# Kernel tuning notes

Measured on AMD Instinct MI355X. Metric: run time of the kernel, lower is better.

## Reference

```python
import jax, jax.numpy as jnp
import numpy as np

N = 100000
E = 1600000
IN_F, HID, OUT_F = 256, 128, 64


def setup_inputs() -> dict:
    key = jax.random.key(0)
    k_x, k_e, k_w1, k_w2, k_b1, k_b2 = jax.random.split(key, 6)
    x = jax.random.normal(k_x, (N, IN_F), dtype=jnp.float32)
    edge_index = jax.random.randint(k_e, (2, E), 0, N, dtype=jnp.int32)
    # GCNConv params: lin has no bias in PyG; separate additive bias per layer.
    W1 = jax.random.normal(k_w1, (IN_F, HID), dtype=jnp.float32) / np.sqrt(IN_F)
    b1 = jax.random.normal(k_b1, (HID,), dtype=jnp.float32) * 0.01
    W2 = jax.random.normal(k_w2, (HID, OUT_F), dtype=jnp.float32) / np.sqrt(HID)
    b2 = jax.random.normal(k_b2, (OUT_F,), dtype=jnp.float32) * 0.01
    return {"x": x, "edge_index": edge_index, "W1": W1, "b1": b1, "W2": W2, "b2": b2}


def _gcn_norm(edge_index, num_nodes):
    # add self loops (improved=False -> weight 1.0), symmetric normalization
    loop = jnp.arange(num_nodes, dtype=edge_index.dtype)
    src = jnp.concatenate([edge_index[0], loop])
    dst = jnp.concatenate([edge_index[1], loop])
    w = jnp.ones(src.shape[0], dtype=jnp.float32)
    deg = jax.ops.segment_sum(w, dst, num_segments=num_nodes)
    dinv = jnp.where(deg > 0, jax.lax.rsqrt(deg), 0.0)
    norm = dinv[src] * w * dinv[dst]
    return src, dst, norm


def _gcn_layer(h, W, b, src, dst, norm, num_nodes):
    h = h @ W                               # [N, out]
    msg = h[src] * norm[:, None]            # [E+N, out] gather + scale
    out = jax.ops.segment_sum(msg, dst, num_segments=num_nodes)  # scatter-add
    return out + b


def reference(x, edge_index, W1, b1, W2, b2):
    # dropout is identity in eval mode
    src, dst, norm = _gcn_norm(edge_index, N)
    h = _gcn_layer(x, W1, b1, src, dst, norm, N)
    h = jax.nn.relu(h)
    out = _gcn_layer(h, W2, b2, src, dst, norm, N)
    return out
```

## Files before the change

### kernel.cpp

```cpp
#include <hip/hip_runtime.h>
#include <hip/hip_bf16.h>

#define N_NODES 100000
#define N_EDGES 1600000
#define IN_FEAT 256
#define HID_F   128
#define OUT_FT  64

#define NBUK   256
#define NPB    391
#define BUKCAP 8192
#define EPB    4096
#define G_BIN  ((N_EDGES + EPB - 1) / EPB)
#define G_GEMM ((N_NODES + 63) / 64)
#define G_CAST ((IN_FEAT * HID_F + HID_F * OUT_FT + 255) / 256)
#define G_AGG  ((N_NODES + 7) / 8)

typedef unsigned short u16;
typedef __attribute__((ext_vector_type(8))) unsigned short u16x8;
typedef __attribute__((ext_vector_type(8))) short short8;
typedef __attribute__((ext_vector_type(4))) float f32x4;

static __device__ inline u16 f2bf(float f) {
    __hip_bfloat16 h = __float2bfloat16(f);
    return *reinterpret_cast<u16*>(&h);
}
static __device__ inline float bf2f(u16 u) {
    union { unsigned u; float f; } c;
    c.u = ((unsigned)u) << 16;
    return c.f;
}


__global__ __launch_bounds__(256) void k_bin(const int* __restrict__ srcA,
                                             const int* __restrict__ dstA,
                                             int* __restrict__ gcur, int2* __restrict__ pairs,
                                             const float* __restrict__ W1,
                                             const float* __restrict__ W2,
                                             u16* __restrict__ W1t, u16* __restrict__ W2t) {
    if (blockIdx.x >= G_BIN) {
        int idx = (blockIdx.x - G_BIN) * 256 + threadIdx.x;
        if (idx < IN_FEAT * HID_F) {
            int k = idx / HID_F, n = idx % HID_F;
            W1t[n * IN_FEAT + k] = f2bf(W1[idx]);
        } else {
            int e2 = idx - IN_FEAT * HID_F;
            if (e2 < HID_F * OUT_FT) {
                int k = e2 / OUT_FT, n = e2 % OUT_FT;
                W2t[n * HID_F + k] = f2bf(W2[e2]);
            }
        }
        return;
    }
    __shared__ int lh[NBUK];
    int t = threadIdx.x;
    int e0 = blockIdx.x * EPB;
    if (t < NBUK) lh[t] = 0;
    __syncthreads();
#pragma unroll
    for (int i = 0; i < EPB / 256; i++) {
        int e = e0 + i * 256 + t;
        if (e < N_EDGES) atomicAdd(&lh[dstA[e] / NPB], 1);
    }
    __syncthreads();
    if (t < NBUK) {
        int c = lh[t];
        lh[t] = atomicAdd(&gcur[t], c);
    }
    __syncthreads();
#pragma unroll
    for (int i = 0; i < EPB / 256; i++) {
        int e = e0 + i * 256 + t;
        if (e < N_EDGES) {
            int d = dstA[e];
            int b = d / NPB;
            int p = atomicAdd(&lh[b], 1);
            if (p < BUKCAP) pairs[(size_t)b * BUKCAP + p] = make_int2(srcA[e], d);
        }
    }
}


__global__ __launch_bounds__(256) void k_fillB(const int2* __restrict__ pairs,
                                               const int* __restrict__ gcnt,
                                               int* __restrict__ offsets,
                                               float* __restrict__ dinv,
                                               int* __restrict__ csr) {
    __shared__ int hist[NPB];
    __shared__ int sm[256];
    __shared__ int s_ebase;
    int b = blockIdx.x, t = threadIdx.x;
    int nbase = b * NPB;
    int nn = min(NPB, N_NODES - nbase);

    int gv = gcnt[t];
    sm[t] = gv;
    __syncthreads();
    for (int o = 1; o < 256; o <<= 1) {
        int u = (t >= o) ? sm[t - o] : 0;
        __syncthreads();
        sm[t] += u;
        __syncthreads();
    }
    if (t == b) s_ebase = sm[t] - gv;
    __syncthreads();
    int ebase = s_ebase;
    int cnt = gcnt[b];
    const int2* pb = pairs + (size_t)b * BUKCAP;

    for (int i = t; i < NPB; i += 256) hist[i] = 0;
    __syncthreads();
    for (int i = t; i < cnt; i += 256) atomicAdd(&hist[pb[i].y - nbase], 1);
    __syncthreads();

    int base2 = t * 2;
    int c0 = (base2 < NPB) ? hist[base2] : 0;
    int c1 = (base2 + 1 < NPB) ? hist[base2 + 1] : 0;
    int s = c0 + c1;
    __syncthreads();
    sm[t] = s;
    __syncthreads();
    for (int o = 1; o < 256; o <<= 1) {
        int u = (t >= o) ? sm[t - o] : 0;
        __syncthreads();
        sm[t] += u;
        __syncthreads();
    }
    int run = ebase + sm[t] - s;
    __syncthreads();
    int cc[2] = {c0, c1};
#pragma unroll
    for (int q = 0; q < 2; q++) {
        int n = base2 + q;
        if (n < nn) {
            int g = nbase + n;
            offsets[g] = run;
            dinv[g] = rsqrtf((float)(cc[q] + 1));
            hist[n] = run;
            run += cc[q];
        }
    }
    __syncthreads();
    for (int i = t; i < cnt; i += 256) {
        int2 e = pb[i];
        int p = atomicAdd(&hist[e.y - nbase], 1);
        csr[p] = e.x;
    }
    if (b == NBUK - 1 && t == 0) offsets[N_NODES] = N_EDGES;
}


__global__ __launch_bounds__(256) void k_gemm1(const float* __restrict__ A,
                                               const u16* __restrict__ Bt,
                                               const float* __restrict__ dinv,
                                               u16* __restrict__ C) {
    __shared__ u16 As[2][64][40];
    __shared__ u16 Bs[2][128][40];
    int tid = threadIdx.x;
    int wv = tid >> 6, lane = tid & 63;
    int m16 = lane & 15, quad = lane >> 4;
    int row0 = blockIdx.x * 64;

    int ar = tid >> 2, aq = tid & 3;
    int br = tid >> 1, bh = tid & 1;
    int arow_g = row0 + ar;
    if (arow_g >= N_NODES) arow_g = N_NODES - 1;
    const float* ap = &A[(size_t)arow_g * IN_FEAT + aq * 8];
    const u16*   bp = &Bt[(size_t)br * IN_FEAT + bh * 16];

    f32x4 acc[8];
#pragma unroll
    for (int j = 0; j < 8; j++) acc[j] = (f32x4)(0.f);

    {
        f32x4 a0 = *(const f32x4*)&ap[0];
        f32x4 a1 = *(const f32x4*)&ap[4];
        u16x8 b0 = *(const u16x8*)&bp[0];
        u16x8 b1 = *(const u16x8*)&bp[8];
        u16x8 av;
#pragma unroll
        for (int j = 0; j < 4; j++) { av[j] = f2bf(a0[j]); av[4 + j] = f2bf(a1[j]); }
        *(u16x8*)&As[0][ar][aq * 8] = av;
        *(u16x8*)&Bs[0][br][bh * 16] = b0;
        *(u16x8*)&Bs[0][br][bh * 16 + 8] = b1;
    }

#pragma unroll
    for (int s = 0; s < 8; s++) {
        const int buf = s & 1;
        f32x4 na0, na1; u16x8 nb0, nb1;
        if (s + 1 < 8) {
            int k0 = (s + 1) * 32;
            na0 = *(const f32x4*)&ap[k0];
            na1 = *(const f32x4*)&ap[k0 + 4];
            nb0 = *(const u16x8*)&bp[k0];
            nb1 = *(const u16x8*)&bp[k0 + 8];
        }
        __syncthreads();
        short8 af = *(const short8*)&As[buf][wv * 16 + m16][quad * 8];
#pragma unroll
        for (int ct = 0; ct < 8; ct++) {
            short8 bf = *(const short8*)&Bs[buf][16 * ct + m16][quad * 8];
            acc[ct] = __builtin_amdgcn_mfma_f32_16x16x32_bf16(af, bf, acc[ct], 0, 0, 0);
        }
        if (s + 1 < 8) {
            u16x8 av;
#pragma unroll
            for (int j = 0; j < 4; j++) { av[j] = f2bf(na0[j]); av[4 + j] = f2bf(na1[j]); }
            *(u16x8*)&As[buf ^ 1][ar][aq * 8] = av;
            *(u16x8*)&Bs[buf ^ 1][br][bh * 16] = nb0;
            *(u16x8*)&Bs[buf ^ 1][br][bh * 16 + 8] = nb1;
        }
    }

#pragma unroll
    for (int r4 = 0; r4 < 4; r4++) {
        int grow = row0 + wv * 16 + quad * 4 + r4;
        if (grow < N_NODES) {
            float dv = dinv[grow];
#pragma unroll
            for (int ct = 0; ct < 8; ct++)
                C[(size_t)grow * HID_F + 16 * ct + m16] = f2bf(acc[ct][r4] * dv);
        }
    }
}


__global__ __launch_bounds__(256) void k_gemm2(const u16* __restrict__ A,
                                               const u16* __restrict__ Bt,
                                               const float* __restrict__ dinv,
                                               u16* __restrict__ C) {
    __shared__ u16 As[2][64][40];
    __shared__ u16 Bs[2][64][40];
    int tid = threadIdx.x;
    int wv = tid >> 6, lane = tid & 63;
    int m16 = lane & 15, quad = lane >> 4;
    int row0 = blockIdx.x * 64;

    int ar = tid >> 2, aq = tid & 3;
    int arow_g = row0 + ar;
    if (arow_g >= N_NODES) arow_g = N_NODES - 1;
    const u16* ap = &A[(size_t)arow_g * HID_F + aq * 8];
    const u16* bp = &Bt[(size_t)ar * HID_F + aq * 8];

    f32x4 acc[4];
#pragma unroll
    for (int j = 0; j < 4; j++) acc[j] = (f32x4)(0.f);

    {
        u16x8 a0 = *(const u16x8*)&ap[0];
        u16x8 b0 = *(const u16x8*)&bp[0];
        *(u16x8*)&As[0][ar][aq * 8] = a0;
        *(u16x8*)&Bs[0][ar][aq * 8] = b0;
    }

#pragma unroll
    for (int s = 0; s < 4; s++) {
        const int buf = s & 1;
        u16x8 na, nb;
        if (s + 1 < 4) {
            int k0 = (s + 1) * 32;
            na = *(const u16x8*)&ap[k0];
            nb = *(const u16x8*)&bp[k0];
        }
        __syncthreads();
        short8 af = *(const short8*)&As[buf][wv * 16 + m16][quad * 8];
#pragma unroll
        for (int ct = 0; ct < 4; ct++) {
            short8 bf = *(const short8*)&Bs[buf][16 * ct + m16][quad * 8];
            acc[ct] = __builtin_amdgcn_mfma_f32_16x16x32_bf16(af, bf, acc[ct], 0, 0, 0);
        }
        if (s + 1 < 4) {
            *(u16x8*)&As[buf ^ 1][ar][aq * 8] = na;
            *(u16x8*)&Bs[buf ^ 1][ar][aq * 8] = nb;
        }
    }

#pragma unroll
    for (int r4 = 0; r4 < 4; r4++) {
        int grow = row0 + wv * 16 + quad * 4 + r4;
        if (grow < N_NODES) {
            float dv = dinv[grow];
#pragma unroll
            for (int ct = 0; ct < 4; ct++)
                C[(size_t)grow * OUT_FT + 16 * ct + m16] = f2bf(acc[ct][r4] * dv);
        }
    }
}


__global__ __launch_bounds__(256) void k_agg1(const u16* __restrict__ hs,
                                              const int* __restrict__ offsets,
                                              const int* __restrict__ csr,
                                              const float* __restrict__ dinv,
                                              const float* __restrict__ b,
                                              u16* __restrict__ out) {
    int wave = threadIdx.x >> 6;
    int lane = threadIdx.x & 63;
    int half = lane >> 5;
    int node = blockIdx.x * 8 + wave * 2 + half;
    if (node >= N_NODES) return;
    int gl = lane & 31;
    int g = gl >> 4;
    int fl = gl & 15;
    const int fo = fl * 8;
    int beg = offsets[node], end = offsets[node + 1];

    float accA[8], accB[8];
#pragma unroll
    for (int i = 0; i < 8; i++) { accA[i] = 0.f; accB[i] = 0.f; }

    int j = beg;
    for (; j + 8 <= end; j += 8) {
        int s0 = csr[j + g];
        int s1 = csr[j + 2 + g];
        int s2 = csr[j + 4 + g];
        int s3 = csr[j + 6 + g];
        u16x8 r0 = *(const u16x8*)&hs[(size_t)s0 * HID_F + fo];
        u16x8 r1 = *(const u16x8*)&hs[(size_t)s1 * HID_F + fo];
        u16x8 r2 = *(const u16x8*)&hs[(size_t)s2 * HID_F + fo];
        u16x8 r3 = *(const u16x8*)&hs[(size_t)s3 * HID_F + fo];
#pragma unroll
        for (int i = 0; i < 8; i++) {
            accA[i] += bf2f(r0[i]) + bf2f(r1[i]);
            accB[i] += bf2f(r2[i]) + bf2f(r3[i]);
        }
    }
    if (j + 4 <= end) {
        int s0 = csr[j + g];
        int s1 = csr[j + 2 + g];
        u16x8 r0 = *(const u16x8*)&hs[(size_t)s0 * HID_F + fo];
        u16x8 r1 = *(const u16x8*)&hs[(size_t)s1 * HID_F + fo];
#pragma unroll
        for (int i = 0; i < 8; i++) accA[i] += bf2f(r0[i]) + bf2f(r1[i]);
        j += 4;
    }
    for (; j < end; j += 2) {
        int idx = j + g;
        if (idx < end) {
            int s = csr[idx];
            u16x8 r0 = *(const u16x8*)&hs[(size_t)s * HID_F + fo];
#pragma unroll
            for (int i = 0; i < 8; i++) accB[i] += bf2f(r0[i]);
        }
    }
#pragma unroll
    for (int i = 0; i < 8; i++) {
        float v = accA[i] + accB[i];
        v += __shfl_xor(v, 16, 64);
        accA[i] = v;
    }
    if (g == 0) {
        u16x8 sr = *(const u16x8*)&hs[(size_t)node * HID_F + fo];
        float dv = dinv[node];
        f32x4 b0 = *(const f32x4*)&b[fo];
        f32x4 b1 = *(const f32x4*)&b[fo + 4];
        u16x8 o;
#pragma unroll
        for (int i = 0; i < 4; i++) {
            o[i]     = f2bf(fmaxf(dv * (accA[i]     + bf2f(sr[i]))     + b0[i], 0.f));
            o[4 + i] = f2bf(fmaxf(dv * (accA[4 + i] + bf2f(sr[4 + i])) + b1[i], 0.f));
        }
        *(u16x8*)&out[(size_t)node * HID_F + fo] = o;
    }
}


__global__ __launch_bounds__(256) void k_agg2(const u16* __restrict__ hs,
                                              const int* __restrict__ offsets,
                                              const int* __restrict__ csr,
                                              const float* __restrict__ dinv,
                                              const float* __restrict__ b,
                                              float* __restrict__ out) {
    int wave = threadIdx.x >> 6;
    int lane = threadIdx.x & 63;
    int half = lane >> 5;
    int node = blockIdx.x * 8 + wave * 2 + half;
    if (node >= N_NODES) return;
    int gl = lane & 31;
    int g = gl >> 3;
    int fl = gl & 7;
    const int fo = fl * 8;
    int beg = offsets[node], end = offsets[node + 1];

    float accA[8], accB[8];
#pragma unroll
    for (int i = 0; i < 8; i++) { accA[i] = 0.f; accB[i] = 0.f; }

    int j = beg;
    for (; j + 16 <= end; j += 16) {
        int s0 = csr[j + g];
        int s1 = csr[j + 4 + g];
        int s2 = csr[j + 8 + g];
        int s3 = csr[j + 12 + g];
        u16x8 r0 = *(const u16x8*)&hs[(size_t)s0 * OUT_FT + fo];
        u16x8 r1 = *(const u16x8*)&hs[(size_t)s1 * OUT_FT + fo];
        u16x8 r2 = *(const u16x8*)&hs[(size_t)s2 * OUT_FT + fo];
        u16x8 r3 = *(const u16x8*)&hs[(size_t)s3 * OUT_FT + fo];
#pragma unroll
        for (int i = 0; i < 8; i++) {
            accA[i] += bf2f(r0[i]) + bf2f(r1[i]);
            accB[i] += bf2f(r2[i]) + bf2f(r3[i]);
        }
    }
    if (j + 8 <= end) {
        int s0 = csr[j + g];
        int s1 = csr[j + 4 + g];
        u16x8 r0 = *(const u16x8*)&hs[(size_t)s0 * OUT_FT + fo];
        u16x8 r1 = *(const u16x8*)&hs[(size_t)s1 * OUT_FT + fo];
#pragma unroll
        for (int i = 0; i < 8; i++) accA[i] += bf2f(r0[i]) + bf2f(r1[i]);
        j += 8;
    }
    for (; j < end; j += 4) {
        int idx = j + g;
        if (idx < end) {
            int s = csr[idx];
            u16x8 r0 = *(const u16x8*)&hs[(size_t)s * OUT_FT + fo];
#pragma unroll
            for (int i = 0; i < 8; i++) accB[i] += bf2f(r0[i]);
        }
    }
#pragma unroll
    for (int i = 0; i < 8; i++) {
        float v = accA[i] + accB[i];
        v += __shfl_xor(v, 8, 64);
        v += __shfl_xor(v, 16, 64);
        accA[i] = v;
    }
    if (g == 0) {
        u16x8 sr = *(const u16x8*)&hs[(size_t)node * OUT_FT + fo];
        float dv = dinv[node];
        f32x4 b0 = *(const f32x4*)&b[fo];
        f32x4 b1 = *(const f32x4*)&b[fo + 4];
        f32x4 o0, o1;
#pragma unroll
        for (int i = 0; i < 4; i++) {
            o0[i] = dv * (accA[i]     + bf2f(sr[i]))     + b0[i];
            o1[i] = dv * (accA[4 + i] + bf2f(sr[4 + i])) + b1[i];
        }
        *(f32x4*)&out[(size_t)node * OUT_FT + fo] = o0;
        *(f32x4*)&out[(size_t)node * OUT_FT + fo + 4] = o1;
    }
}


extern "C" void kernel_launch(void* const* d_in, const int* in_sizes, int n_in,
                              void* d_out, int out_size, void* d_ws, size_t ws_size,
                              hipStream_t stream) {
    const float* x  = (const float*)d_in[0];
    const int*   ei = (const int*)d_in[1];
    const float* W1 = (const float*)d_in[2];
    const float* b1 = (const float*)d_in[3];
    const float* W2 = (const float*)d_in[4];
    const float* b2 = (const float*)d_in[5];
    float* out = (float*)d_out;

    char* ws = (char*)d_ws;
    int*   offsets = (int*)(ws + 0);
    float* dinv    = (float*)(ws + 400512);
    int*   csr     = (int*)(ws + 800512);
    u16*   W1t     = (u16*)(ws + 7200512);
    u16*   W2t     = (u16*)(ws + 7266048);
    int*   gcur    = (int*)(ws + 7282432);
    u16*   hs1     = (u16*)(ws + 7284608);
    u16*   a1      = (u16*)(ws + 32884608);
    int2*  pairs   = (int2*)(ws + 32884608);
    u16*   hs2     = hs1;

    const int* srcA = ei;
    const int* dstA = ei + N_EDGES;

    hipMemsetAsync(gcur, 0, NBUK * sizeof(int), stream);

    k_bin<<<G_BIN + G_CAST, 256, 0, stream>>>(srcA, dstA, gcur, pairs, W1, W2, W1t, W2t);
    k_fillB<<<NBUK, 256, 0, stream>>>(pairs, gcur, offsets, dinv, csr);

    k_gemm1<<<G_GEMM, 256, 0, stream>>>(x, W1t, dinv, hs1);
    k_agg1<<<G_AGG, 256, 0, stream>>>(hs1, offsets, csr, dinv, b1, a1);
    k_gemm2<<<G_GEMM, 256, 0, stream>>>(a1, W2t, dinv, hs2);
    k_agg2<<<G_AGG, 256, 0, stream>>>(hs2, offsets, csr, dinv, b2, out);
}
```

Before: 338.2 us.

## Fuse layer-1 aggregation with layer-2 GEMM via shared-memory tile

```diff
diff --git a/kernel.cpp b/kernel.cpp
--- a/kernel.cpp
+++ b/kernel.cpp
@@ -226,53 +226,107 @@
 }
 
 
-__global__ __launch_bounds__(256) void k_gemm2(const u16* __restrict__ A,
-                                               const u16* __restrict__ Bt,
-                                               const float* __restrict__ dinv,
-                                               u16* __restrict__ C) {
-    __shared__ u16 As[2][64][40];
-    __shared__ u16 Bs[2][64][40];
-    int tid = threadIdx.x;
-    int wv = tid >> 6, lane = tid & 63;
-    int m16 = lane & 15, quad = lane >> 4;
+__global__ __launch_bounds__(256) void k_agg1gemm2(const u16* __restrict__ hs,
+                                                   const int* __restrict__ offsets,
+                                                   const int* __restrict__ csr,
+                                                   const float* __restrict__ dinv,
+                                                   const float* __restrict__ b1v,
+                                                   const u16* __restrict__ W2t,
+                                                   u16* __restrict__ hs2) {
+    __shared__ u16 As[4][65][40];
+    int t = threadIdx.x;
+    int wave = t >> 6;
+    int lane = t & 63;
+    int half = lane >> 5;
     int row0 = blockIdx.x * 64;
 
-    int ar = tid >> 2, aq = tid & 3;
-    int arow_g = row0 + ar;
-    if (arow_g >= N_NODES) arow_g = N_NODES - 1;
-    const u16* ap = &A[(size_t)arow_g * HID_F + aq * 8];
-    const u16* bp = &Bt[(size_t)ar * HID_F + aq * 8];
-
+    int gl = lane & 31;
+    int g = gl >> 4;
+    int fl = gl & 15;
+    const int fo = fl * 8;
+
+#pragma unroll 1
+    for (int sweep = 0; sweep < 8; sweep++) {
+        int nl = sweep * 8 + wave * 2 + half;
+        int node = row0 + nl;
+        if (node < N_NODES) {
+            int beg = offsets[node], end = offsets[node + 1];
+
+            float accA[8], accB[8];
+#pragma unroll
+            for (int i = 0; i < 8; i++) { accA[i] = 0.f; accB[i] = 0.f; }
+
+            int j = beg;
+            for (; j + 8 <= end; j += 8) {
+                int s0 = csr[j + g];
+                int s1 = csr[j + 2 + g];
+                int s2 = csr[j + 4 + g];
+                int s3 = csr[j + 6 + g];
+                u16x8 r0 = *(const u16x8*)&hs[(size_t)s0 * HID_F + fo];
+                u16x8 r1 = *(const u16x8*)&hs[(size_t)s1 * HID_F + fo];
+                u16x8 r2 = *(const u16x8*)&hs[(size_t)s2 * HID_F + fo];
+                u16x8 r3 = *(const u16x8*)&hs[(size_t)s3 * HID_F + fo];
+#pragma unroll
+                for (int i = 0; i < 8; i++) {
+                    accA[i] += bf2f(r0[i]) + bf2f(r1[i]);
+                    accB[i] += bf2f(r2[i]) + bf2f(r3[i]);
+                }
+            }
+            if (j + 4 <= end) {
+                int s0 = csr[j + g];
+                int s1 = csr[j + 2 + g];
+                u16x8 r0 = *(const u16x8*)&hs[(size_t)s0 * HID_F + fo];
+                u16x8 r1 = *(const u16x8*)&hs[(size_t)s1 * HID_F + fo];
+#pragma unroll
+                for (int i = 0; i < 8; i++) accA[i] += bf2f(r0[i]) + bf2f(r1[i]);
+                j += 4;
+            }
+            for (; j < end; j += 2) {
+                int idx = j + g;
+                if (idx < end) {
+                    int s = csr[idx];
+                    u16x8 r0 = *(const u16x8*)&hs[(size_t)s * HID_F + fo];
+#pragma unroll
+                    for (int i = 0; i < 8; i++) accB[i] += bf2f(r0[i]);
+                }
+            }
+#pragma unroll
+            for (int i = 0; i < 8; i++) {
+                float v = accA[i] + accB[i];
+                v += __shfl_xor(v, 16, 64);
+                accA[i] = v;
+            }
+            if (g == 0) {
+                u16x8 sr = *(const u16x8*)&hs[(size_t)node * HID_F + fo];
+                float dv = dinv[node];
+                f32x4 b0 = *(const f32x4*)&b1v[fo];
+                f32x4 b1q = *(const f32x4*)&b1v[fo + 4];
+                u16x8 o;
+#pragma unroll
+                for (int i = 0; i < 4; i++) {
+                    o[i]     = f2bf(fmaxf(dv * (accA[i]     + bf2f(sr[i]))     + b0[i], 0.f));
+                    o[4 + i] = f2bf(fmaxf(dv * (accA[4 + i] + bf2f(sr[4 + i])) + b1q[i], 0.f));
+                }
+                int c = fo >> 5;
+                int off = fo & 31;
+                *(u16x8*)&As[c][nl][off] = o;
+            }
+        }
+    }
+    __syncthreads();
+
+    int wv = wave, m16 = lane & 15, quad = lane >> 4;
     f32x4 acc[4];
 #pragma unroll
     for (int j = 0; j < 4; j++) acc[j] = (f32x4)(0.f);
 
-    {
-        u16x8 a0 = *(const u16x8*)&ap[0];
-        u16x8 b0 = *(const u16x8*)&bp[0];
-        *(u16x8*)&As[0][ar][aq * 8] = a0;
-        *(u16x8*)&Bs[0][ar][aq * 8] = b0;
-    }
-
 #pragma unroll
     for (int s = 0; s < 4; s++) {
-        const int buf = s & 1;
-        u16x8 na, nb;
-        if (s + 1 < 4) {
-            int k0 = (s + 1) * 32;
-            na = *(const u16x8*)&ap[k0];
-            nb = *(const u16x8*)&bp[k0];
-        }
-        __syncthreads();
-        short8 af = *(const short8*)&As[buf][wv * 16 + m16][quad * 8];
+        short8 af = *(const short8*)&As[s][wv * 16 + m16][quad * 8];
 #pragma unroll
         for (int ct = 0; ct < 4; ct++) {
-            short8 bf = *(const short8*)&Bs[buf][16 * ct + m16][quad * 8];
+            short8 bf = *(const short8*)&W2t[(size_t)(16 * ct + m16) * HID_F + s * 32 + quad * 8];
             acc[ct] = __builtin_amdgcn_mfma_f32_16x16x32_bf16(af, bf, acc[ct], 0, 0, 0);
-        }
-        if (s + 1 < 4) {
-            *(u16x8*)&As[buf ^ 1][ar][aq * 8] = na;
-            *(u16x8*)&Bs[buf ^ 1][ar][aq * 8] = nb;
         }
     }
 
@@ -283,85 +337,8 @@
             float dv = dinv[grow];
 #pragma unroll
             for (int ct = 0; ct < 4; ct++)
-                C[(size_t)grow * OUT_FT + 16 * ct + m16] = f2bf(acc[ct][r4] * dv);
-        }
-    }
-}
-
-
-__global__ __launch_bounds__(256) void k_agg1(const u16* __restrict__ hs,
-                                              const int* __restrict__ offsets,
-                                              const int* __restrict__ csr,
-                                              const float* __restrict__ dinv,
-                                              const float* __restrict__ b,
-                                              u16* __restrict__ out) {
-    int wave = threadIdx.x >> 6;
-    int lane = threadIdx.x & 63;
-    int half = lane >> 5;
-    int node = blockIdx.x * 8 + wave * 2 + half;
-    if (node >= N_NODES) return;
-    int gl = lane & 31;
-    int g = gl >> 4;
-    int fl = gl & 15;
-    const int fo = fl * 8;
-    int beg = offsets[node], end = offsets[node + 1];
-
-    float accA[8], accB[8];
-#pragma unroll
-    for (int i = 0; i < 8; i++) { accA[i] = 0.f; accB[i] = 0.f; }
-
-    int j = beg;
-    for (; j + 8 <= end; j += 8) {
-        int s0 = csr[j + g];
-        int s1 = csr[j + 2 + g];
-        int s2 = csr[j + 4 + g];
-        int s3 = csr[j + 6 + g];
-        u16x8 r0 = *(const u16x8*)&hs[(size_t)s0 * HID_F + fo];
-        u16x8 r1 = *(const u16x8*)&hs[(size_t)s1 * HID_F + fo];
-        u16x8 r2 = *(const u16x8*)&hs[(size_t)s2 * HID_F + fo];
-        u16x8 r3 = *(const u16x8*)&hs[(size_t)s3 * HID_F + fo];
-#pragma unroll
-        for (int i = 0; i < 8; i++) {
-            accA[i] += bf2f(r0[i]) + bf2f(r1[i]);
-            accB[i] += bf2f(r2[i]) + bf2f(r3[i]);
-        }
-    }
-    if (j + 4 <= end) {
-        int s0 = csr[j + g];
-        int s1 = csr[j + 2 + g];
-        u16x8 r0 = *(const u16x8*)&hs[(size_t)s0 * HID_F + fo];
-        u16x8 r1 = *(const u16x8*)&hs[(size_t)s1 * HID_F + fo];
-#pragma unroll
-        for (int i = 0; i < 8; i++) accA[i] += bf2f(r0[i]) + bf2f(r1[i]);
-        j += 4;
-    }
-    for (; j < end; j += 2) {
-        int idx = j + g;
-        if (idx < end) {
-            int s = csr[idx];
-            u16x8 r0 = *(const u16x8*)&hs[(size_t)s * HID_F + fo];
-#pragma unroll
-            for (int i = 0; i < 8; i++) accB[i] += bf2f(r0[i]);
-        }
-    }
-#pragma unroll
-    for (int i = 0; i < 8; i++) {
-        float v = accA[i] + accB[i];
-        v += __shfl_xor(v, 16, 64);
-        accA[i] = v;
-    }
-    if (g == 0) {
-        u16x8 sr = *(const u16x8*)&hs[(size_t)node * HID_F + fo];
-        float dv = dinv[node];
-        f32x4 b0 = *(const f32x4*)&b[fo];
-        f32x4 b1 = *(const f32x4*)&b[fo + 4];
-        u16x8 o;
-#pragma unroll
-        for (int i = 0; i < 4; i++) {
-            o[i]     = f2bf(fmaxf(dv * (accA[i]     + bf2f(sr[i]))     + b0[i], 0.f));
-            o[4 + i] = f2bf(fmaxf(dv * (accA[4 + i] + bf2f(sr[4 + i])) + b1[i], 0.f));
-        }
-        *(u16x8*)&out[(size_t)node * HID_F + fo] = o;
+                hs2[(size_t)grow * OUT_FT + 16 * ct + m16] = f2bf(acc[ct][r4] * dv);
+        }
     }
 }
 
@@ -464,9 +441,8 @@
     u16*   W2t     = (u16*)(ws + 7266048);
     int*   gcur    = (int*)(ws + 7282432);
     u16*   hs1     = (u16*)(ws + 7284608);
-    u16*   a1      = (u16*)(ws + 32884608);
+    u16*   hs2     = (u16*)(ws + 32884608);
     int2*  pairs   = (int2*)(ws + 32884608);
-    u16*   hs2     = hs1;
 
     const int* srcA = ei;
     const int* dstA = ei + N_EDGES;
@@ -477,7 +453,6 @@
     k_fillB<<<NBUK, 256, 0, stream>>>(pairs, gcur, offsets, dinv, csr);
 
     k_gemm1<<<G_GEMM, 256, 0, stream>>>(x, W1t, dinv, hs1);
-    k_agg1<<<G_AGG, 256, 0, stream>>>(hs1, offsets, csr, dinv, b1, a1);
-    k_gemm2<<<G_GEMM, 256, 0, stream>>>(a1, W2t, dinv, hs2);
+    k_agg1gemm2<<<G_GEMM, 256, 0, stream>>>(hs1, offsets, csr, dinv, b1, W2t, hs2);
     k_agg2<<<G_AGG, 256, 0, stream>>>(hs2, offsets, csr, dinv, b2, out);
 }
```

After: 359.8 us. 6.4% more time.
